# Optimization experiments

Hardware: AMD Instinct MI355X
Metric: run time of the kernel (lower is better)

## Reference

```python
import jax, jax.numpy as jnp
from jax import lax
import numpy as np

D_MODEL = 1024; N_HEADS = 16; D_K = 64; D_FF = 4096
D_STATE = 16; D_CONV = 4; D_INNER = 2048; EPS = 1e-5
BATCH = 2; SEQ = 2048


def _ln(x, g, b):
    m = x.mean(-1, keepdims=True)
    v = ((x - m) ** 2).mean(-1, keepdims=True)
    return (x - m) * lax.rsqrt(v + EPS) * g + b


def setup_inputs() -> dict:
    key = jax.random.key(0)
    ks = jax.random.split(key, 12)
    rn = lambda k, sh, s=0.02: jax.random.normal(k, sh, jnp.float32) * s
    return {
        'x': jax.random.normal(ks[0], (BATCH, SEQ, D_MODEL), jnp.float32),
        'ln1_g': jnp.ones(D_MODEL), 'ln1_b': jnp.zeros(D_MODEL),
        'Wq': rn(ks[1], (D_MODEL, D_MODEL)), 'bq': jnp.zeros(D_MODEL),
        'Wk': rn(ks[2], (D_MODEL, D_MODEL)), 'bk': jnp.zeros(D_MODEL),
        'Wv': rn(ks[3], (D_MODEL, D_MODEL)), 'bv': jnp.zeros(D_MODEL),
        'Wo': rn(ks[4], (D_MODEL, D_MODEL)), 'bo': jnp.zeros(D_MODEL),
        'ln2_g': jnp.ones(D_MODEL), 'ln2_b': jnp.zeros(D_MODEL),
        'in_w': rn(ks[5], (D_MODEL, 2 * D_INNER)), 'in_b': jnp.zeros(2 * D_INNER),
        'conv_w': rn(ks[6], (D_INNER, 1, D_CONV), 0.2), 'conv_b': jnp.zeros(D_INNER),
        'xp_w': rn(ks[7], (D_INNER, 2 * D_STATE)), 'xp_b': jnp.zeros(2 * D_STATE),
        'dt': rn(ks[8], (D_INNER,), 0.1), 'A': rn(ks[9], (D_STATE, D_STATE), 0.1),
        'Dp': jnp.ones(D_INNER),
        'out_w': rn(ks[10], (D_INNER, D_MODEL)), 'out_b': jnp.zeros(D_MODEL),
        'ln3_g': jnp.ones(D_MODEL), 'ln3_b': jnp.zeros(D_MODEL),
        'fc1_w': rn(ks[11], (D_MODEL, D_FF)), 'fc1_b': jnp.zeros(D_FF),
        'fc2_w': rn(jax.random.fold_in(key, 99), (D_FF, D_MODEL)), 'fc2_b': jnp.zeros(D_MODEL),
    }


def reference(x, ln1_g, ln1_b, Wq, bq, Wk, bk, Wv, bv, Wo, bo, ln2_g, ln2_b,
              in_w, in_b, conv_w, conv_b, xp_w, xp_b, dt, A, Dp, out_w, out_b,
              ln3_g, ln3_b, fc1_w, fc1_b, fc2_w, fc2_b):
    Bsz, S, _ = x.shape
    # --- attention (block sliding-window mask == full causal mask) ---
    h = _ln(x, ln1_g, ln1_b)
    q = (h @ Wq + bq).reshape(Bsz, S, N_HEADS, D_K).transpose(0, 2, 1, 3)
    k = (h @ Wk + bk).reshape(Bsz, S, N_HEADS, D_K).transpose(0, 2, 1, 3)
    v = (h @ Wv + bv).reshape(Bsz, S, N_HEADS, D_K).transpose(0, 2, 1, 3)
    scores = jnp.einsum('bhqd,bhkd->bhqk', q, k) / float(D_K ** 0.5)
    causal = jnp.tril(jnp.ones((S, S), bool))
    scores = jnp.where(causal, scores, -jnp.inf)
    probs = jax.nn.softmax(scores, axis=-1)
    attn = jnp.einsum('bhqk,bhkd->bhqd', probs, v).transpose(0, 2, 1, 3).reshape(Bsz, S, D_MODEL)
    x = x + attn @ Wo + bo
    # --- Mamba-style layer ---
    h = _ln(x, ln2_g, ln2_b)
    xr = h @ in_w + in_b                      # (B,S,2*Di)
    xm, res = xr[..., :D_INNER], xr[..., D_INNER:]
    # causal depthwise conv: torch Conv1d(pad=d_conv-1)[..., :S] == left-pad conv
    xc = lax.conv_general_dilated(xm.transpose(0, 2, 1), conv_w, (1,), [(D_CONV - 1, 0)],
                                  dimension_numbers=('NCH', 'OIH', 'NCH'),
                                  feature_group_count=D_INNER)
    xm = jax.nn.silu((xc + conv_b[None, :, None]).transpose(0, 2, 1))
    xdbl = xm @ xp_w + xp_b                   # (B,S,2*d_state)
    Bm, Cm = xdbl[..., :D_STATE], xdbl[..., D_STATE:]
    # dt = exp(param)[:d_state], indexed by i % d_state per step (as in source)
    dts = jnp.exp(dt)[:D_STATE][jnp.arange(S) % D_STATE]  # (S,)
    # NOTE: the source scan never uses u = x[:,i,:] (and hence D); hs depends
    # only on dt, A, B, C — replicated faithfully here.

    def step(hst, inp):
        d_t, b_t, c_t = inp
        A_t = jnp.exp(d_t * A)                # (d_state,d_state)
        hst = jnp.tanh(hst @ A_t.T) + b_t * hst + c_t
        return hst, hst

    h0 = jnp.zeros((Bsz, D_STATE), x.dtype)
    _, hs = lax.scan(step, h0, (dts, Bm.transpose(1, 0, 2), Cm.transpose(1, 0, 2)))
    hs = hs.transpose(1, 0, 2)                # (B,S,d_state)
    y = jnp.repeat(hs, D_INNER // D_STATE, axis=-1) + res
    x = x + y @ out_w + out_b
    # --- FFN (tanh-approx GELU) ---
    h = _ln(x, ln3_g, ln3_b)
    x = x + jax.nn.gelu(h @ fc1_w + fc1_b, approximate=True) @ fc2_w + fc2_b
    return x
```

## Files before the change

kernel.cpp:

```cpp
#include <hip/hip_runtime.h>
#include <hip/hip_bf16.h>


#define SEQ     2048
#define BATCH   2
#define MROWS   4096
#define DMODEL  1024
#define DINNER  2048
#define DFF     4096
#define QKVLD   3072

typedef __attribute__((ext_vector_type(8))) short bf16x8;
typedef __attribute__((ext_vector_type(4))) float f32x4;
typedef __attribute__((ext_vector_type(2))) __fp16 f16x2;

__device__ __forceinline__ unsigned short f2b(float x){
    __hip_bfloat16 h = __float2bfloat16(x);
    return *reinterpret_cast<unsigned short*>(&h);
}
__device__ __forceinline__ float b2f(unsigned short u){
    __hip_bfloat16 h;
    *reinterpret_cast<unsigned short*>(&h) = u;
    return __bfloat162float(h);
}
__device__ __forceinline__ float gelu_f(float v){
    float u = 0.7978845608f*(v + 0.044715f*v*v*v);
    float e = __expf(2.f*u);
    float th = 1.f - 2.f*__builtin_amdgcn_rcpf(e + 1.f);
    return 0.5f*v*(1.f + th);
}
__device__ __forceinline__ void gload16(const unsigned short* g, unsigned short* l){
    __builtin_amdgcn_global_load_lds(
        (const __attribute__((address_space(1))) void*)g,
        (__attribute__((address_space(3))) void*)l, 16, 0, 0);
}
template<int CTRL>
__device__ __forceinline__ float dppf(float x){
    int r = __builtin_amdgcn_mov_dpp(__builtin_bit_cast(int, x), CTRL, 0xf, 0xf, false);
    return __builtin_bit_cast(float, r);
}
template<int CTRL>
__device__ __forceinline__ int dppi(int x){
    return __builtin_amdgcn_mov_dpp(x, CTRL, 0xf, 0xf, false);
}
template<int CTRL>
__device__ __forceinline__ f16x2 dpp_h2(f16x2 x){
    int r = __builtin_amdgcn_mov_dpp(__builtin_bit_cast(int, x), CTRL, 0xf, 0xf, false);
    return __builtin_bit_cast(f16x2, r);
}

#if __has_builtin(__builtin_amdgcn_exp2f)
#define W_SCALE 2.8853900817779268f
__device__ __forceinline__ float exp_2s(float x){ return __builtin_amdgcn_exp2f(x); }
#else
#define W_SCALE 2.0f
__device__ __forceinline__ float exp_2s(float x){ return __expf(x); }
#endif

__device__ __forceinline__ float hdot2(f16x2 a, f16x2 b, float c){
#if __has_builtin(__builtin_amdgcn_fdot2)
    return __builtin_amdgcn_fdot2(a, b, c, false);
#else
    return c + (float)a[0]*(float)b[0] + (float)a[1]*(float)b[1];
#endif
}

__global__ __launch_bounds__(256) void transpose_cast(
    const float* __restrict__ W, unsigned short* __restrict__ Wt, int K, int N)
{
    __shared__ float t[64*65];
    int n0 = blockIdx.x*64, k0 = blockIdx.y*64;
    int c = threadIdx.x & 63, r0 = threadIdx.x >> 6;
    #pragma unroll
    for (int rr = 0; rr < 64; rr += 4)
        t[(rr+r0)*65 + c] = W[(size_t)(k0+rr+r0)*N + n0 + c];
    __syncthreads();
    #pragma unroll
    for (int rr = 0; rr < 64; rr += 4)
        Wt[(size_t)(n0+rr+r0)*K + k0 + c] = f2b(t[c*65 + rr + r0]);
}

__global__ __launch_bounds__(256) void concat_bias(
    const float* __restrict__ b0, const float* __restrict__ b1,
    const float* __restrict__ b2, float* __restrict__ o)
{
    int t = blockIdx.x*256 + threadIdx.x;
    float v = (t < 1024) ? b0[t] : (t < 2048 ? b1[t-1024] : b2[t-2048]);
    o[t] = v;
}

__global__ __launch_bounds__(256) void layernorm_bf16(
    const float* __restrict__ x, const float* __restrict__ g,
    const float* __restrict__ b, unsigned short* __restrict__ out)
{
    int row = blockIdx.x;
    const float4* xr = (const float4*)(x + (size_t)row*DMODEL);
    int tid = threadIdx.x;
    float4 xv = xr[tid];
    float s  = xv.x + xv.y + xv.z + xv.w;
    float ss = xv.x*xv.x + xv.y*xv.y + xv.z*xv.z + xv.w*xv.w;
    #pragma unroll
    for (int d = 32; d > 0; d >>= 1){ s += __shfl_xor(s,d); ss += __shfl_xor(ss,d); }
    __shared__ float sm[8];
    int wv = tid>>6, ln = tid&63;
    if (ln == 0){ sm[wv] = s; sm[4+wv] = ss; }
    __syncthreads();
    s  = sm[0]+sm[1]+sm[2]+sm[3];
    ss = sm[4]+sm[5]+sm[6]+sm[7];
    float mean = s*(1.f/DMODEL);
    float var  = ss*(1.f/DMODEL) - mean*mean;
    float rstd = rsqrtf(var + 1e-5f);
    float4 gv = ((const float4*)g)[tid];
    float4 bv = ((const float4*)b)[tid];
    ushort4 o;
    o.x = f2b((xv.x-mean)*rstd*gv.x + bv.x);
    o.y = f2b((xv.y-mean)*rstd*gv.y + bv.y);
    o.z = f2b((xv.z-mean)*rstd*gv.z + bv.z);
    o.w = f2b((xv.w-mean)*rstd*gv.w + bv.w);
    ((ushort4*)(out + (size_t)row*DMODEL))[tid] = o;
}

template<int BN, int OUT_BF16, int HAS_RES, int ACT>
__global__ __launch_bounds__(256,2) void gemm_bt(
    const unsigned short* __restrict__ A, const unsigned short* __restrict__ Bt,
    const float* __restrict__ bias, const float* __restrict__ res,
    void* __restrict__ outp, int Ndim, int Kdim)
{
    constexpr int NT = BN/32;
    constexpr int BROWS = BN/32;
    __shared__ unsigned short As[128*64];
    __shared__ unsigned short Bs[BN*64];
    int tid = threadIdx.x;
    int lane = tid & 63, wv = tid >> 6;
    int l15 = lane & 15, quad = lane >> 4;
    int m0 = blockIdx.y*128, n0 = blockIdx.x*BN;
    int mo = (wv>>1)*64, no = (wv&1)*(BN/2);
    int rsub = (lane >> 3);
    int cc8  = (lane & 7)*8;
    f32x4 zz = {0.f,0.f,0.f,0.f};
    f32x4 acc[4][NT];
    #pragma unroll
    for (int i=0;i<4;++i)
      #pragma unroll
      for (int j=0;j<NT;++j) acc[i][j] = zz;

    for (int k0 = 0; k0 < Kdim; k0 += 64){
        const unsigned short* Ab = A  + (size_t)(m0 + wv*32 + rsub)*Kdim + k0 + cc8;
        const unsigned short* Bb = Bt + (size_t)(n0 + wv*(BN/4) + rsub)*Kdim + k0 + cc8;
        #pragma unroll
        for (int i=0;i<4;++i)
            gload16(Ab + (size_t)(i*8)*Kdim, &As[(wv*32 + i*8)*64]);
        #pragma unroll
        for (int i=0;i<BROWS;++i)
            gload16(Bb + (size_t)(i*8)*Kdim, &Bs[(wv*(BN/4) + i*8)*64]);
        __syncthreads();
        #pragma unroll
        for (int kc=0;kc<2;++kc){
            bf16x8 af[4], bfr[NT];
            #pragma unroll
            for (int t=0;t<4;++t)
                af[t]  = *(const bf16x8*)(&As[(mo + t*16 + l15)*64 + kc*32 + quad*8]);
            #pragma unroll
            for (int t=0;t<NT;++t)
                bfr[t] = *(const bf16x8*)(&Bs[(no + t*16 + l15)*64 + kc*32 + quad*8]);
            #pragma unroll
            for (int mt=0;mt<4;++mt)
              #pragma unroll
              for (int nt=0;nt<NT;++nt)
                acc[mt][nt] = __builtin_amdgcn_mfma_f32_16x16x32_bf16(af[mt], bfr[nt], acc[mt][nt], 0,0,0);
        }
        __syncthreads();
    }
    #pragma unroll
    for (int mt=0;mt<4;++mt){
      #pragma unroll
      for (int nt=0;nt<NT;++nt){
        int gn = n0 + no + nt*16 + l15;
        float bval = bias[gn];
        #pragma unroll
        for (int r=0;r<4;++r){
            int gm = m0 + mo + mt*16 + quad*4 + r;
            size_t off = (size_t)gm*Ndim + gn;
            float v = acc[mt][nt][r] + bval;
            if constexpr (HAS_RES) v += res[off];
            if constexpr (ACT == 1) v = gelu_f(v);
            if constexpr (OUT_BF16) ((unsigned short*)outp)[off] = f2b(v);
            else                    ((float*)outp)[off] = v;
        }
      }
    }
}

__global__ __launch_bounds__(256,2) void attn_flash(
    const unsigned short* __restrict__ qkv, unsigned short* __restrict__ attn)
{
    __shared__ unsigned short Qs[64*72];
    __shared__ unsigned short Ks[64*72];
    __shared__ unsigned short Vt[64*72];
    __shared__ unsigned short Ps[64*72];
    int bh = blockIdx.y;
    int qt = (int)gridDim.x - 1 - (int)blockIdx.x;
    int q0 = qt*64;
    int tid = threadIdx.x, wv = tid>>6, lane = tid&63;
    int l15 = lane&15, quad = lane>>4;
    const size_t basei = (size_t)(bh>>4)*SEQ*QKVLD + (size_t)(bh&15)*64;
    const unsigned short* q = qkv + basei;
    const unsigned short* k = qkv + basei + DMODEL;
    const unsigned short* v = qkv + basei + 2*DMODEL;
    const size_t baseo = (size_t)(bh>>4)*SEQ*DMODEL + (size_t)(bh&15)*64;

    #pragma unroll
    for (int i=0;i<2;++i){
        int cch = tid + i*256; int r = cch>>3, cc = cch&7;
        *(uint4*)(&Qs[r*72 + cc*8]) = *(const uint4*)(q + (size_t)(q0+r)*QKVLD + cc*8);
    }
    __syncthreads();
    bf16x8 aq0 = *(const bf16x8*)(&Qs[(wv*16 + l15)*72 + quad*8]);
    bf16x8 aq1 = *(const bf16x8*)(&Qs[(wv*16 + l15)*72 + 32 + quad*8]);

    float m_i[4], l_i[4];
    f32x4 zz = {0.f,0.f,0.f,0.f};
    f32x4 o[4];
    #pragma unroll
    for (int r=0;r<4;++r){ m_i[r] = -__builtin_inff(); l_i[r] = 0.f; }
    #pragma unroll
    for (int d=0;d<4;++d) o[d] = zz;

    for (int kt = 0; kt <= qt; ++kt){
        int t0 = kt*64;
        #pragma unroll
        for (int i=0;i<2;++i){
            int cch = tid + i*256; int r = cch>>3, cc = cch&7;
            *(uint4*)(&Ks[r*72 + cc*8]) = *(const uint4*)(k + (size_t)(t0+r)*QKVLD + cc*8);
            uint4 vv = *(const uint4*)(v + (size_t)(t0+r)*QKVLD + cc*8);
            const unsigned short* pv = (const unsigned short*)&vv;
            #pragma unroll
            for (int j=0;j<8;++j) Vt[(cc*8+j)*72 + r] = pv[j];
        }
        __syncthreads();

        f32x4 sc[4];
        #pragma unroll
        for (int st=0;st<4;++st){
            bf16x8 b0 = *(const bf16x8*)(&Ks[(st*16+l15)*72 + quad*8]);
            bf16x8 b1 = *(const bf16x8*)(&Ks[(st*16+l15)*72 + 32 + quad*8]);
            sc[st] = __builtin_amdgcn_mfma_f32_16x16x32_bf16(aq0, b0, zz, 0,0,0);
            sc[st] = __builtin_amdgcn_mfma_f32_16x16x32_bf16(aq1, b1, sc[st], 0,0,0);
        }
        bool diag = (kt == qt);
        float sval[4][4];
        float mrow[4];
        #pragma unroll
        for (int r=0;r<4;++r) mrow[r] = -__builtin_inff();
        #pragma unroll
        for (int st=0;st<4;++st)
          #pragma unroll
          for (int r=0;r<4;++r){
            float svv = sc[st][r]*0.125f;
            if (diag && (st*16 + l15 > wv*16 + quad*4 + r)) svv = -__builtin_inff();
            sval[st][r] = svv;
            mrow[r] = fmaxf(mrow[r], svv);
          }
        #pragma unroll
        for (int d=1; d<16; d<<=1)
          #pragma unroll
          for (int r=0;r<4;++r) mrow[r] = fmaxf(mrow[r], __shfl_xor(mrow[r], d));
        float alpha[4], rsum[4];
        #pragma unroll
        for (int r=0;r<4;++r){
            float mn = fmaxf(m_i[r], mrow[r]);
            alpha[r] = __expf(m_i[r] - mn);
            m_i[r] = mn;
        }
        #pragma unroll
        for (int st=0;st<4;++st)
          #pragma unroll
          for (int r=0;r<4;++r) sval[st][r] = __expf(sval[st][r] - m_i[r]);
        #pragma unroll
        for (int r=0;r<4;++r) rsum[r] = sval[0][r]+sval[1][r]+sval[2][r]+sval[3][r];
        #pragma unroll
        for (int d=1; d<16; d<<=1)
          #pragma unroll
          for (int r=0;r<4;++r) rsum[r] += __shfl_xor(rsum[r], d);
        #pragma unroll
        for (int r=0;r<4;++r) l_i[r] = l_i[r]*alpha[r] + rsum[r];
        #pragma unroll
        for (int st=0;st<4;++st)
          #pragma unroll
          for (int r=0;r<4;++r)
            Ps[(wv*16 + quad*4 + r)*72 + st*16 + l15] = f2b(sval[st][r]);
        #pragma unroll
        for (int d=0;d<4;++d)
          #pragma unroll
          for (int r=0;r<4;++r) o[d][r] = o[d][r]*alpha[r];
        __syncthreads();
        bf16x8 ap0 = *(const bf16x8*)(&Ps[(wv*16 + l15)*72 + quad*8]);
        bf16x8 ap1 = *(const bf16x8*)(&Ps[(wv*16 + l15)*72 + 32 + quad*8]);
        #pragma unroll
        for (int dtile=0;dtile<4;++dtile){
            bf16x8 b0 = *(const bf16x8*)(&Vt[(dtile*16+l15)*72 + quad*8]);
            bf16x8 b1 = *(const bf16x8*)(&Vt[(dtile*16+l15)*72 + 32 + quad*8]);
            o[dtile] = __builtin_amdgcn_mfma_f32_16x16x32_bf16(ap0, b0, o[dtile], 0,0,0);
            o[dtile] = __builtin_amdgcn_mfma_f32_16x16x32_bf16(ap1, b1, o[dtile], 0,0,0);
        }
        __syncthreads();
    }
    #pragma unroll
    for (int r=0;r<4;++r){
        float inv = 1.f/l_i[r];
        int gm = q0 + wv*16 + quad*4 + r;
        #pragma unroll
        for (int dtile=0;dtile<4;++dtile)
            attn[baseo + (size_t)gm*DMODEL + dtile*16 + l15] = f2b(o[dtile][r]*inv);
    }
}

__global__ __launch_bounds__(256) void conv_silu(
    const unsigned short* __restrict__ xr, const float* __restrict__ cw,
    const float* __restrict__ cb, unsigned short* __restrict__ xm2)
{
    int idx = blockIdx.x*256 + threadIdx.x;
    int r  = idx >> 10;
    int c2 = (idx & 1023)*2;
    int s  = r & (SEQ-1);
    float4 w0 = *(const float4*)(cw + c2*4);
    float4 w1 = *(const float4*)(cw + (c2+1)*4);
    float w0a[4] = {w0.x,w0.y,w0.z,w0.w};
    float w1a[4] = {w1.x,w1.y,w1.z,w1.w};
    float a0 = cb[c2], a1 = cb[c2+1];
    const unsigned short* xrow = xr + (size_t)r*DFF + c2;
    #pragma unroll
    for (int j=0;j<4;++j){
        int sp = s - 3 + j;
        if (sp >= 0){
            int off = (j-3)*DFF;
            unsigned int u = *(const unsigned int*)(xrow + off);
            a0 += w0a[j]*b2f(u & 0xffff);
            a1 += w1a[j]*b2f(u >> 16);
        }
    }
    float s0 = a0 * __builtin_amdgcn_rcpf(1.f + __expf(-a0));
    float s1 = a1 * __builtin_amdgcn_rcpf(1.f + __expf(-a1));
    unsigned int op = (unsigned int)f2b(s0) | ((unsigned int)f2b(s1) << 16);
    *(unsigned int*)(xm2 + (size_t)r*DINNER + c2) = op;
}

__global__ __launch_bounds__(256) void xp_gemm(
    const unsigned short* __restrict__ xm2, const float* __restrict__ w,
    const float* __restrict__ bias, float* __restrict__ xdbl)
{
    int tid = threadIdx.x;
    int lr = tid >> 5, n = tid & 31;
    int row = blockIdx.x*8 + lr;
    const unsigned short* ar = xm2 + (size_t)row*DINNER;
    float acc = bias[n];
    #pragma unroll 4
    for (int k2 = 0; k2 < DINNER; k2 += 2){
        unsigned int u = *(const unsigned int*)(ar + k2);
        acc += b2f(u & 0xffff)*w[k2*32 + n] + b2f(u >> 16)*w[(k2+1)*32 + n];
    }
    int nc = (n < 16) ? 2*n : 2*(n-16)+1;
    xdbl[(size_t)row*32 + nc] = acc;
}

__device__ __forceinline__ float scan_step_dot(float h, const f16x2 (&Wp)[8],
                                               float bv, float cv)
{
    float rr = dppf<0x121>(h);
    f16x2 p0 = __builtin_amdgcn_cvt_pkrtz(h, rr);
    f16x2 p1 = dpp_h2<0x122>(p0);
    f16x2 p2 = dpp_h2<0x124>(p0);
    f16x2 p3 = dpp_h2<0x126>(p0);
    f16x2 p4 = dpp_h2<0x128>(p0);
    f16x2 p5 = dpp_h2<0x12a>(p0);
    f16x2 p6 = dpp_h2<0x12c>(p0);
    f16x2 p7 = dpp_h2<0x12e>(p0);
    float a0 = hdot2(Wp[0], p0, 0.f);
    a0 = hdot2(Wp[1], p1, a0);
    a0 = hdot2(Wp[2], p2, a0);
    a0 = hdot2(Wp[3], p3, a0);
    float a1 = hdot2(Wp[4], p4, 0.f);
    a1 = hdot2(Wp[5], p5, a1);
    a1 = hdot2(Wp[6], p6, a1);
    a1 = hdot2(Wp[7], p7, a1);
    float u  = fmaf(bv, h, cv + 1.f);
    float e2 = exp_2s(a0 + a1);
    float r  = __builtin_amdgcn_rcpf(e2 + 1.f);
    return fmaf(-2.f, r, u);
}

__device__ __forceinline__ void load_bank(float2 (&bk)[16], const float* src){
    #pragma unroll
    for (int j=0;j<16;++j) bk[j] = *(const float2*)(src + (size_t)j*32);
}

__device__ __forceinline__ void compute16(const float2 (&bk)[16],
                                          const f16x2 (&Wf)[16][8],
                                          float& hn, float* hp, int lane)
{
    float h0s=0.f, h1s=0.f, h2s=0.f;
    #pragma unroll
    for (int j=0;j<16;++j){
        hn = scan_step_dot(hn, Wf[j], bk[j].x, bk[j].y);
        if ((j&3)==0)      h0s = hn;
        else if ((j&3)==1) h1s = hn;
        else if ((j&3)==2) h2s = hn;
        else if (lane < 16){
            float4 o4 = {h0s, h1s, h2s, hn};
            *(float4*)(hp + j - 3) = o4;
        }
    }
}

__global__ __launch_bounds__(128,1) void scan_k(
    const float* __restrict__ xdbl, const float* __restrict__ dt,
    const float* __restrict__ A, float* __restrict__ hsT)
{
    int tid = threadIdx.x;
    int lane = tid & 63;
    int b = tid >> 6;
    int i = lane & 15;

    int c1 = dppi<0x121>(i);
    int sj[8], tj[8];
    sj[0] = i;               tj[0] = c1;
    sj[1] = dppi<0x122>(i);  tj[1] = dppi<0x122>(c1);
    sj[2] = dppi<0x124>(i);  tj[2] = dppi<0x124>(c1);
    sj[3] = dppi<0x126>(i);  tj[3] = dppi<0x126>(c1);
    sj[4] = dppi<0x128>(i);  tj[4] = dppi<0x128>(c1);
    sj[5] = dppi<0x12a>(i);  tj[5] = dppi<0x12a>(c1);
    sj[6] = dppi<0x12c>(i);  tj[6] = dppi<0x12c>(c1);
    sj[7] = dppi<0x12e>(i);  tj[7] = dppi<0x12e>(c1);

    f16x2 Wf[16][8];
    #pragma unroll
    for (int p=0;p<16;++p){
        float dtp = __expf(dt[p]);
        #pragma unroll
        for (int jj=0;jj<8;++jj){
            float w0 = W_SCALE*__expf(dtp * A[i*16 + sj[jj]]);
            float w1 = W_SCALE*__expf(dtp * A[i*16 + tj[jj]]);
            Wf[p][jj] = __builtin_amdgcn_cvt_pkrtz(w0, w1);
        }
    }

    const float* src = xdbl + (size_t)(b*SEQ)*32 + 2*i;
    float* hp = hsT + (size_t)(b*16 + i)*SEQ;
    float2 bA[16], bB[16];
    load_bank(bA, src);
    float hn = 0.f;
    for (int bp = 0; bp < 64; ++bp){
        int t0 = bp*32;
        load_bank(bB, src + (size_t)(t0+16)*32);
        compute16(bA, Wf, hn, hp + t0, lane);
        int t2 = (bp < 63) ? (t0 + 32) : 0;
        load_bank(bA, src + (size_t)t2*32);
        compute16(bB, Wf, hn, hp + t0 + 16, lane);
    }
}

__global__ __launch_bounds__(256) void y_assemble(
    const float* __restrict__ hsT, const unsigned short* __restrict__ xr,
    unsigned short* __restrict__ y)
{
    int idx = blockIdx.x*256 + threadIdx.x;
    int r = idx >> 10;
    int c2 = (idx & 1023)*2;
    int bb = r >> 11, s = r & (SEQ-1);
    unsigned int u = *(const unsigned int*)(xr + (size_t)r*DFF + DINNER + c2);
    float h0 = hsT[(size_t)(bb*16 + (c2 >> 7))*SEQ + s];
    float y0 = h0 + b2f(u & 0xffff);
    float y1 = h0 + b2f(u >> 16);
    *(unsigned int*)(y + (size_t)r*DINNER + c2) =
        (unsigned int)f2b(y0) | ((unsigned int)f2b(y1) << 16);
}

extern "C" void kernel_launch(void* const* d_in, const int* in_sizes, int n_in,
                              void* d_out, int out_size, void* d_ws, size_t ws_size,
                              hipStream_t stream)
{
    (void)in_sizes; (void)n_in; (void)out_size; (void)ws_size;
    const float* x     = (const float*)d_in[0];
    const float* ln1_g = (const float*)d_in[1];
    const float* ln1_b = (const float*)d_in[2];
    const float* Wq    = (const float*)d_in[3];
    const float* bq    = (const float*)d_in[4];
    const float* Wk    = (const float*)d_in[5];
    const float* bk    = (const float*)d_in[6];
    const float* Wv    = (const float*)d_in[7];
    const float* bv    = (const float*)d_in[8];
    const float* Wo    = (const float*)d_in[9];
    const float* bo    = (const float*)d_in[10];
    const float* ln2_g = (const float*)d_in[11];
    const float* ln2_b = (const float*)d_in[12];
    const float* in_w  = (const float*)d_in[13];
    const float* in_b  = (const float*)d_in[14];
    const float* conv_w= (const float*)d_in[15];
    const float* conv_b= (const float*)d_in[16];
    const float* xp_w  = (const float*)d_in[17];
    const float* xp_b  = (const float*)d_in[18];
    const float* dt    = (const float*)d_in[19];
    const float* A     = (const float*)d_in[20];
    const float* out_w = (const float*)d_in[22];
    const float* out_b = (const float*)d_in[23];
    const float* ln3_g = (const float*)d_in[24];
    const float* ln3_b = (const float*)d_in[25];
    const float* fc1_w = (const float*)d_in[26];
    const float* fc1_b = (const float*)d_in[27];
    const float* fc2_w = (const float*)d_in[28];
    const float* fc2_b = (const float*)d_in[29];

    char* ws = (char*)d_ws;
    const size_t MB = 1ull << 20;
    unsigned short* qkvT = (unsigned short*)(ws + 0*MB);
    unsigned short* WoT  = (unsigned short*)(ws + 6*MB);
    unsigned short* inT  = (unsigned short*)(ws + 8*MB);
    unsigned short* outT = (unsigned short*)(ws + 16*MB);
    unsigned short* f1T  = (unsigned short*)(ws + 20*MB);
    unsigned short* f2T  = (unsigned short*)(ws + 28*MB);
    unsigned short* hbf  = (unsigned short*)(ws + 36*MB);
    float*          x2   = (float*)(ws + 44*MB);
    float*          x3   = (float*)(ws + 60*MB);
    unsigned short* qkv  = (unsigned short*)(ws + 76*MB);
    unsigned short* attnb= (unsigned short*)(ws + 100*MB);
    unsigned short* xr   = (unsigned short*)(ws + 76*MB);
    unsigned short* ffn  = (unsigned short*)(ws + 76*MB);
    unsigned short* xm2  = (unsigned short*)(ws + 108*MB);
    unsigned short* yb   = (unsigned short*)(ws + 108*MB);
    float*          xdbl = (float*)(ws + 124*MB);
    float*          hsb  = (float*)(ws + 124*MB + 512*1024);
    float*          bqkv = (float*)(ws + 125*MB);

    dim3 blk(256);
    transpose_cast<<<dim3(16,16), blk, 0, stream>>>(Wq, qkvT,              1024, 1024);
    transpose_cast<<<dim3(16,16), blk, 0, stream>>>(Wk, qkvT + 1024*1024,  1024, 1024);
    transpose_cast<<<dim3(16,16), blk, 0, stream>>>(Wv, qkvT + 2*1024*1024,1024, 1024);
    transpose_cast<<<dim3(16,16), blk, 0, stream>>>(Wo, WoT, 1024, 1024);
    transpose_cast<<<dim3(64,16), blk, 0, stream>>>(in_w, inT, 1024, 4096);
    transpose_cast<<<dim3(16,32), blk, 0, stream>>>(out_w, outT, 2048, 1024);
    transpose_cast<<<dim3(64,16), blk, 0, stream>>>(fc1_w, f1T, 1024, 4096);
    transpose_cast<<<dim3(16,64), blk, 0, stream>>>(fc2_w, f2T, 4096, 1024);
    concat_bias<<<12, blk, 0, stream>>>(bq, bk, bv, bqkv);

    layernorm_bf16<<<MROWS, blk, 0, stream>>>(x, ln1_g, ln1_b, hbf);
    gemm_bt<128,1,0,0><<<dim3(24,32), blk, 0, stream>>>(hbf, qkvT, bqkv, nullptr, qkv, QKVLD, 1024);
    attn_flash<<<dim3(32,32), blk, 0, stream>>>(qkv, attnb);
    gemm_bt<64,0,1,0><<<dim3(16,32), blk, 0, stream>>>(attnb, WoT, bo, x, x2, 1024, 1024);
    layernorm_bf16<<<MROWS, blk, 0, stream>>>(x2, ln2_g, ln2_b, hbf);
    gemm_bt<128,1,0,0><<<dim3(32,32), blk, 0, stream>>>(hbf, inT, in_b, nullptr, xr, 4096, 1024);
    conv_silu<<<16384, blk, 0, stream>>>(xr, conv_w, conv_b, xm2);
    xp_gemm<<<512, blk, 0, stream>>>(xm2, xp_w, xp_b, xdbl);
    scan_k<<<1, dim3(128), 0, stream>>>(xdbl, dt, A, hsb);
    y_assemble<<<16384, blk, 0, stream>>>(hsb, xr, yb);
    gemm_bt<64,0,1,0><<<dim3(16,32), blk, 0, stream>>>(yb, outT, out_b, x2, x3, 1024, 2048);
    layernorm_bf16<<<MROWS, blk, 0, stream>>>(x3, ln3_g, ln3_b, hbf);
    gemm_bt<128,1,0,1><<<dim3(32,32), blk, 0, stream>>>(hbf, f1T, fc1_b, nullptr, ffn, 4096, 1024);
    gemm_bt<64,0,1,0><<<dim3(16,32), blk, 0, stream>>>(ffn, f2T, fc2_b, x3, (float*)d_out, 1024, 4096);
}
```

Measured before the change: 930.3 us.

## Pre-transpose V and double-buffer 128-key tiles in flash attention

```diff
diff --git a/kernel.cpp b/kernel.cpp
--- a/kernel.cpp
+++ b/kernel.cpp
@@ -30,6 +30,11 @@
     return 0.5f*v*(1.f + th);
 }
 __device__ __forceinline__ void gload16(const unsigned short* g, unsigned short* l){
+    __builtin_amdgcn_global_load_lds(
+        (const __attribute__((address_space(1))) void*)g,
+        (__attribute__((address_space(3))) void*)l, 16, 0, 0);
+}
+__device__ __forceinline__ void gload16f(const float* g, float* l){
     __builtin_amdgcn_global_load_lds(
         (const __attribute__((address_space(1))) void*)g,
         (__attribute__((address_space(3))) void*)l, 16, 0, 0);
@@ -191,13 +196,51 @@
     }
 }
 
+__global__ __launch_bounds__(256) void transpose_v(
+    const unsigned short* __restrict__ qkv, unsigned short* __restrict__ vT)
+{
+    __shared__ unsigned int t[64*33];
+    int bh = blockIdx.y;
+    int t0 = blockIdx.x*64;
+    int tid = threadIdx.x;
+    const size_t base = (size_t)(bh>>4)*SEQ*QKVLD + (size_t)(bh&15)*64 + 2*DMODEL;
+    #pragma unroll
+    for (int i=0;i<2;++i){
+        int idx = tid + i*256;
+        int r = idx>>3, cc = idx&7;
+        uint4 vv = *(const uint4*)(qkv + base + (size_t)(t0+r)*QKVLD + cc*8);
+        t[r*33 + cc*4 + 0] = vv.x;
+        t[r*33 + cc*4 + 1] = vv.y;
+        t[r*33 + cc*4 + 2] = vv.z;
+        t[r*33 + cc*4 + 3] = vv.w;
+    }
+    __syncthreads();
+    unsigned short* outb = vT + (size_t)bh*64*SEQ + t0;
+    #pragma unroll
+    for (int i=0;i<2;++i){
+        int idx = tid + i*256;
+        int d = idx>>3, cc = idx&7;
+        int sh = (d&1)*16, dp = d>>1;
+        unsigned int o4[4];
+        #pragma unroll
+        for (int j2=0;j2<4;++j2){
+            unsigned int ua = t[(cc*8 + 2*j2    )*33 + dp];
+            unsigned int ub = t[(cc*8 + 2*j2 + 1)*33 + dp];
+            unsigned int ha = (ua >> sh) & 0xffff;
+            unsigned int hb = (ub >> sh) & 0xffff;
+            o4[j2] = ha | (hb << 16);
+        }
+        *(uint4*)(outb + (size_t)d*SEQ + cc*8) = *(uint4*)o4;
+    }
+}
+
 __global__ __launch_bounds__(256,2) void attn_flash(
-    const unsigned short* __restrict__ qkv, unsigned short* __restrict__ attn)
-{
-    __shared__ unsigned short Qs[64*72];
-    __shared__ unsigned short Ks[64*72];
-    __shared__ unsigned short Vt[64*72];
-    __shared__ unsigned short Ps[64*72];
+    const unsigned short* __restrict__ qkv, const unsigned short* __restrict__ vT,
+    unsigned short* __restrict__ attn)
+{
+    __shared__ unsigned short Ks[128*72];
+    __shared__ unsigned short Vt[64*136];
+    __shared__ unsigned short Ps[64*136];
     int bh = blockIdx.y;
     int qt = (int)gridDim.x - 1 - (int)blockIdx.x;
     int q0 = qt*64;
@@ -206,17 +249,21 @@
     const size_t basei = (size_t)(bh>>4)*SEQ*QKVLD + (size_t)(bh&15)*64;
     const unsigned short* q = qkv + basei;
     const unsigned short* k = qkv + basei + DMODEL;
-    const unsigned short* v = qkv + basei + 2*DMODEL;
+    const unsigned short* vTb = vT + (size_t)bh*64*SEQ;
     const size_t baseo = (size_t)(bh>>4)*SEQ*DMODEL + (size_t)(bh&15)*64;
 
-    #pragma unroll
-    for (int i=0;i<2;++i){
-        int cch = tid + i*256; int r = cch>>3, cc = cch&7;
-        *(uint4*)(&Qs[r*72 + cc*8]) = *(const uint4*)(q + (size_t)(q0+r)*QKVLD + cc*8);
-    }
-    __syncthreads();
-    bf16x8 aq0 = *(const bf16x8*)(&Qs[(wv*16 + l15)*72 + quad*8]);
-    bf16x8 aq1 = *(const bf16x8*)(&Qs[(wv*16 + l15)*72 + 32 + quad*8]);
+    bf16x8 aq0 = *(const bf16x8*)(q + (size_t)(q0 + wv*16 + l15)*QKVLD + quad*8);
+    bf16x8 aq1 = *(const bf16x8*)(q + (size_t)(q0 + wv*16 + l15)*QKVLD + 32 + quad*8);
+
+    int nkt = (q0 + 191) >> 7;
+
+    uint4 rK[4], rV[4];
+    #pragma unroll
+    for (int p=0;p<4;++p){
+        int c = tid + p*256;
+        rK[p] = *(const uint4*)(k   + (size_t)(c>>3)*QKVLD + (c&7)*8);
+        rV[p] = *(const uint4*)(vTb + (size_t)(c>>4)*SEQ   + (c&15)*8);
+    }
 
     float m_i[4], l_i[4];
     f32x4 zz = {0.f,0.f,0.f,0.f};
@@ -226,39 +273,46 @@
     #pragma unroll
     for (int d=0;d<4;++d) o[d] = zz;
 
-    for (int kt = 0; kt <= qt; ++kt){
-        int t0 = kt*64;
-        #pragma unroll
-        for (int i=0;i<2;++i){
-            int cch = tid + i*256; int r = cch>>3, cc = cch&7;
-            *(uint4*)(&Ks[r*72 + cc*8]) = *(const uint4*)(k + (size_t)(t0+r)*QKVLD + cc*8);
-            uint4 vv = *(const uint4*)(v + (size_t)(t0+r)*QKVLD + cc*8);
-            const unsigned short* pv = (const unsigned short*)&vv;
+    for (int kt = 0; kt < nkt; ++kt){
+        int t0 = kt*128;
+        __syncthreads();
+        #pragma unroll
+        for (int p=0;p<4;++p){
+            int c = tid + p*256;
+            *(uint4*)(&Ks[(c>>3)*72  + (c&7)*8])  = rK[p];
+            *(uint4*)(&Vt[(c>>4)*136 + (c&15)*8]) = rV[p];
+        }
+        __syncthreads();
+        if (kt + 1 < nkt){
+            int t1 = t0 + 128;
             #pragma unroll
-            for (int j=0;j<8;++j) Vt[(cc*8+j)*72 + r] = pv[j];
-        }
-        __syncthreads();
-
-        f32x4 sc[4];
-        #pragma unroll
-        for (int st=0;st<4;++st){
+            for (int p=0;p<4;++p){
+                int c = tid + p*256;
+                rK[p] = *(const uint4*)(k   + (size_t)(t1 + (c>>3))*QKVLD + (c&7)*8);
+                rV[p] = *(const uint4*)(vTb + (size_t)(c>>4)*SEQ + t1 + (c&15)*8);
+            }
+        }
+
+        f32x4 sc[8];
+        #pragma unroll
+        for (int st=0;st<8;++st){
             bf16x8 b0 = *(const bf16x8*)(&Ks[(st*16+l15)*72 + quad*8]);
             bf16x8 b1 = *(const bf16x8*)(&Ks[(st*16+l15)*72 + 32 + quad*8]);
             sc[st] = __builtin_amdgcn_mfma_f32_16x16x32_bf16(aq0, b0, zz, 0,0,0);
             sc[st] = __builtin_amdgcn_mfma_f32_16x16x32_bf16(aq1, b1, sc[st], 0,0,0);
         }
-        bool diag = (kt == qt);
-        float sval[4][4];
+        bool diagt = (kt == nkt-1);
         float mrow[4];
         #pragma unroll
         for (int r=0;r<4;++r) mrow[r] = -__builtin_inff();
         #pragma unroll
-        for (int st=0;st<4;++st)
+        for (int st=0;st<8;++st)
           #pragma unroll
           for (int r=0;r<4;++r){
             float svv = sc[st][r]*0.125f;
-            if (diag && (st*16 + l15 > wv*16 + quad*4 + r)) svv = -__builtin_inff();
-            sval[st][r] = svv;
+            if (diagt && (t0 + st*16 + l15 > q0 + wv*16 + quad*4 + r))
+                svv = -__builtin_inff();
+            sc[st][r] = svv;
             mrow[r] = fmaxf(mrow[r], svv);
           }
         #pragma unroll
@@ -273,11 +327,14 @@
             m_i[r] = mn;
         }
         #pragma unroll
-        for (int st=0;st<4;++st)
+        for (int st=0;st<8;++st)
           #pragma unroll
-          for (int r=0;r<4;++r) sval[st][r] = __expf(sval[st][r] - m_i[r]);
-        #pragma unroll
-        for (int r=0;r<4;++r) rsum[r] = sval[0][r]+sval[1][r]+sval[2][r]+sval[3][r];
+          for (int r=0;r<4;++r) sc[st][r] = __expf(sc[st][r] - m_i[r]);
+        #pragma unroll
+        for (int r=0;r<4;++r){
+            rsum[r] = ((sc[0][r]+sc[1][r])+(sc[2][r]+sc[3][r]))
+                    + ((sc[4][r]+sc[5][r])+(sc[6][r]+sc[7][r]));
+        }
         #pragma unroll
         for (int d=1; d<16; d<<=1)
           #pragma unroll
@@ -285,25 +342,27 @@
         #pragma unroll
         for (int r=0;r<4;++r) l_i[r] = l_i[r]*alpha[r] + rsum[r];
         #pragma unroll
-        for (int st=0;st<4;++st)
+        for (int st=0;st<8;++st)
           #pragma unroll
           for (int r=0;r<4;++r)
-            Ps[(wv*16 + quad*4 + r)*72 + st*16 + l15] = f2b(sval[st][r]);
+            Ps[(wv*16 + quad*4 + r)*136 + st*16 + l15] = f2b(sc[st][r]);
         #pragma unroll
         for (int d=0;d<4;++d)
           #pragma unroll
           for (int r=0;r<4;++r) o[d][r] = o[d][r]*alpha[r];
-        __syncthreads();
-        bf16x8 ap0 = *(const bf16x8*)(&Ps[(wv*16 + l15)*72 + quad*8]);
-        bf16x8 ap1 = *(const bf16x8*)(&Ps[(wv*16 + l15)*72 + 32 + quad*8]);
+
+        bf16x8 ap[4];
+        #pragma unroll
+        for (int kch=0;kch<4;++kch)
+            ap[kch] = *(const bf16x8*)(&Ps[(wv*16 + l15)*136 + kch*32 + quad*8]);
         #pragma unroll
         for (int dtile=0;dtile<4;++dtile){
-            bf16x8 b0 = *(const bf16x8*)(&Vt[(dtile*16+l15)*72 + quad*8]);
-            bf16x8 b1 = *(const bf16x8*)(&Vt[(dtile*16+l15)*72 + 32 + quad*8]);
-            o[dtile] = __builtin_amdgcn_mfma_f32_16x16x32_bf16(ap0, b0, o[dtile], 0,0,0);
-            o[dtile] = __builtin_amdgcn_mfma_f32_16x16x32_bf16(ap1, b1, o[dtile], 0,0,0);
-        }
-        __syncthreads();
+            #pragma unroll
+            for (int kch=0;kch<4;++kch){
+                bf16x8 bv_ = *(const bf16x8*)(&Vt[(dtile*16+l15)*136 + kch*32 + quad*8]);
+                o[dtile] = __builtin_amdgcn_mfma_f32_16x16x32_bf16(ap[kch], bv_, o[dtile], 0,0,0);
+            }
+        }
     }
     #pragma unroll
     for (int r=0;r<4;++r){
@@ -544,7 +603,8 @@
 
     layernorm_bf16<<<MROWS, blk, 0, stream>>>(x, ln1_g, ln1_b, hbf);
     gemm_bt<128,1,0,0><<<dim3(24,32), blk, 0, stream>>>(hbf, qkvT, bqkv, nullptr, qkv, QKVLD, 1024);
-    attn_flash<<<dim3(32,32), blk, 0, stream>>>(qkv, attnb);
+    transpose_v<<<dim3(32,32), blk, 0, stream>>>(qkv, hbf);
+    attn_flash<<<dim3(32,32), blk, 0, stream>>>(qkv, hbf, attnb);
     gemm_bt<64,0,1,0><<<dim3(16,32), blk, 0, stream>>>(attnb, WoT, bo, x, x2, 1024, 1024);
     layernorm_bf16<<<MROWS, blk, 0, stream>>>(x2, ln2_g, ln2_b, hbf);
     gemm_bt<128,1,0,0><<<dim3(32,32), blk, 0, stream>>>(hbf, inT, in_b, nullptr, xr, 4096, 1024);
```

After: 938.7 us. About the same (+0.9%).
